# Optimization experiments

Hardware: AMD Instinct MI355X
Metric: run time of the kernel (lower is better)

The kernel has to match this reference:

```python
import jax, jax.numpy as jnp
import numpy as np

N_NODES = 50000
N_EDGES = 640000
DIM_V = 128
DIM_E = 128
BN_EPS = 1e-5


def _lrelu(x):
    return jax.nn.leaky_relu(x, 0.2)


def _mlp3(x, W1, b1, W2, b2, W3, b3):
    h = _lrelu(x @ W1 + b1)
    h = _lrelu(h @ W2 + b2)
    return h @ W3 + b3


def _bn_train(x, gamma, beta):
    # BatchNorm1d in training mode: batch stats, biased variance
    m = jnp.mean(x, axis=0)
    v = jnp.mean((x - m) ** 2, axis=0)
    return (x - m) * jax.lax.rsqrt(v + BN_EPS) * gamma + beta


def setup_inputs() -> dict:
    key = jax.random.key(0)
    ks = jax.random.split(key, 20)
    node_fea = jax.random.normal(ks[0], (N_NODES, DIM_V), dtype=jnp.float32)
    edge_fea = jax.random.normal(ks[1], (N_EDGES, DIM_E), dtype=jnp.float32)
    idx1 = jax.random.randint(ks[2], (N_EDGES,), 0, N_NODES)
    idx2 = jax.random.randint(ks[3], (N_EDGES,), 0, N_NODES)
    dt_e = 2 * DIM_V + DIM_E  # phi_e input dim
    dt_v = DIM_V + DIM_E      # phi_v input dim
    s = 0.05
    return {
        "node_fea": node_fea, "edge_fea": edge_fea,
        "idx1": idx1, "idx2": idx2,
        "We1": jax.random.normal(ks[4], (dt_e, DIM_E), jnp.float32) * s,
        "be1": jnp.zeros((DIM_E,), jnp.float32),
        "We2": jax.random.normal(ks[5], (DIM_E, DIM_E), jnp.float32) * s,
        "be2": jnp.zeros((DIM_E,), jnp.float32),
        "We3": jax.random.normal(ks[6], (DIM_E, DIM_E), jnp.float32) * s,
        "be3": jnp.zeros((DIM_E,), jnp.float32),
        "Wv1": jax.random.normal(ks[7], (dt_v, DIM_V), jnp.float32) * s,
        "bv1": jnp.zeros((DIM_V,), jnp.float32),
        "Wv2": jax.random.normal(ks[8], (DIM_V, DIM_V), jnp.float32) * s,
        "bv2": jnp.zeros((DIM_V,), jnp.float32),
        "Wv3": jax.random.normal(ks[9], (DIM_V, DIM_V), jnp.float32) * s,
        "bv3": jnp.zeros((DIM_V,), jnp.float32),
        "gamma_e": jnp.ones((DIM_E,), jnp.float32),
        "beta_e": jnp.zeros((DIM_E,), jnp.float32),
        "gamma_v": jnp.ones((DIM_V,), jnp.float32),
        "beta_v": jnp.zeros((DIM_V,), jnp.float32),
    }


def reference(node_fea, edge_fea, idx1, idx2,
              We1, be1, We2, be2, We3, be3,
              Wv1, bv1, Wv2, bv2, Wv3, bv3,
              gamma_e, beta_e, gamma_v, beta_v):
    n_nodes = node_fea.shape[0]
    # gather endpoints, concat with edge features -> [E, 2*dim_v + dim_e]
    z = jnp.concatenate([node_fea[idx1], node_fea[idx2], edge_fea], axis=1)
    ek_prime = _bn_train(_mlp3(z, We1, be1, We2, be2, We3, be3), gamma_e, beta_e)
    edge_new = edge_fea + ek_prime
    # scatter_mean over idx1 into [N, dim_v]; empty segments stay zero
    seg_sum = jax.ops.segment_sum(ek_prime, idx1, num_segments=n_nodes)
    cnt = jax.ops.segment_sum(jnp.ones((idx1.shape[0], 1), ek_prime.dtype), idx1,
                              num_segments=n_nodes)
    vi_e_bar = seg_sum / jnp.maximum(cnt, 1.0)
    z2 = jnp.concatenate([vi_e_bar, node_fea], axis=1)
    vi_prime = _bn_train(_mlp3(z2, Wv1, bv1, Wv2, bv2, Wv3, bv3), gamma_v, beta_v)
    node_new = node_fea + vi_prime
    return node_new, edge_new
```

## Files before the change

### kernel.cpp

```cpp
#include <hip/hip_runtime.h>
#include <cstddef>

#define BN_EPS 1e-5f
constexpr int NNODES = 50000;
constexpr int NEDGES = 640000;
constexpr int DV = 128;
constexpr int NSLOT_E = 512;
constexpr int NSLOT_V = 256;

typedef __attribute__((ext_vector_type(4))) float f32x4;
typedef __attribute__((ext_vector_type(8))) short s16x8;
typedef unsigned short ushort_t;

__device__ __forceinline__ float lrelu(float x) { return x > 0.f ? x : 0.2f * x; }

__device__ __forceinline__ unsigned cvt_pk_bf16(float lo, float hi) {
  unsigned r;
  asm("v_cvt_pk_bf16_f32 %0, %1, %2" : "=v"(r) : "v"(lo), "v"(hi));
  return r;
}
__device__ __forceinline__ ushort_t f2bf(float f) {
  unsigned r;
  asm("v_cvt_pk_bf16_f32 %0, %1, %1" : "=v"(r) : "v"(f));
  return (ushort_t)r;
}
__device__ __forceinline__ s16x8 pack8(float4 a, float4 b) {
  union { unsigned u[4]; s16x8 v; } r;
  r.u[0] = cvt_pk_bf16(a.x, a.y);
  r.u[1] = cvt_pk_bf16(a.z, a.w);
  r.u[2] = cvt_pk_bf16(b.x, b.y);
  r.u[3] = cvt_pk_bf16(b.z, b.w);
  return r.v;
}
__device__ __forceinline__ float bf2f(ushort_t u) {
  return __builtin_bit_cast(float, (unsigned int)u << 16);
}

__global__ __launch_bounds__(256)
void to_bf16(const float* __restrict__ src, ushort_t* __restrict__ dst, int n8) {
  int i = blockIdx.x * 256 + threadIdx.x;
  if (i >= n8) return;
  const float* s = src + (size_t)i * 8;
  float4 x0 = *(const float4*)s;
  float4 x1 = *(const float4*)(s + 4);
  *(s16x8*)(dst + (size_t)i * 8) = pack8(x0, x1);
}

__global__ __launch_bounds__(256)
void pack_all(const float* __restrict__ W0, const float* __restrict__ W1,
              const float* __restrict__ W2, const float* __restrict__ W3,
              const float* __restrict__ W4, const float* __restrict__ W5,
              ushort_t* __restrict__ out) {
  int t = blockIdx.x * 256 + threadIdx.x;
  if (t >= 288 * 64) return;
  int lane = t & 63, f = t >> 6;
  const float* W; int lf;
  if (f < 96)       { W = W0; lf = f; }
  else if (f < 128) { W = W1; lf = f - 96; }
  else if (f < 160) { W = W2; lf = f - 128; }
  else if (f < 224) { W = W3; lf = f - 160; }
  else if (f < 256) { W = W4; lf = f - 224; }
  else              { W = W5; lf = f - 256; }
  int kk = lf >> 3, n = lf & 7;
  int k0 = kk * 32 + (lane >> 4) * 8, col = n * 16 + (lane & 15);
  s16x8 v;
#pragma unroll
  for (int j = 0; j < 8; j++) v[j] = (short)f2bf(W[(size_t)(k0 + j) * DV + col]);
  *(s16x8*)(out + (size_t)t * 8) = v;
}

__global__ __launch_bounds__(256)
void csr_hist(const int* __restrict__ idx1, int* __restrict__ deg) {
  int e = blockIdx.x * 256 + threadIdx.x;
  if (e < NEDGES) atomicAdd(&deg[idx1[e]], 1);
}

__global__ __launch_bounds__(256)
void csr_scan(const int* __restrict__ deg, int* __restrict__ row_ptr,
              int* __restrict__ cursor) {
  __shared__ int part[256];
  const int t = threadIdx.x;
  const int CH = (NNODES + 255) / 256;
  int s = 0;
  for (int i = 0; i < CH; i++) { int n = t * CH + i; if (n < NNODES) s += deg[n]; }
  part[t] = s;
  __syncthreads();
  if (t == 0) {
    int run = 0;
    for (int i = 0; i < 256; i++) { int v = part[i]; part[i] = run; run += v; }
  }
  __syncthreads();
  int run = part[t];
  for (int i = 0; i < CH; i++) {
    int n = t * CH + i;
    if (n < NNODES) { row_ptr[n] = run; cursor[n] = run; run += deg[n]; }
  }
}

__global__ __launch_bounds__(256)
void csr_fill(const int* __restrict__ idx1, int* __restrict__ cursor,
              int* __restrict__ eidx) {
  int e = blockIdx.x * 256 + threadIdx.x;
  if (e < NEDGES) {
    int pos = atomicAdd(&cursor[idx1[e]], 1);
    eidx[pos] = e;
  }
}

template<int RS>
__device__ __forceinline__ void mfma_span(const char* Als, const s16x8* __restrict__ Wp,
                                          int fkk0, int nkk, f32x4 acc[2][2],
                                          int lane, int rg, int nh) {
  const int col0 = lane & 15;
  const int kg16 = (lane >> 4) * 16;
  const int sw = (col0 & 7) << 4;
  const int r0 = (rg * 32 + col0) * RS;
  const int r1 = (rg * 32 + 16 + col0) * RS;
#pragma unroll
  for (int kk = 0; kk < nkk; kk++) {
    const int ko = (kk * 64 + kg16) ^ sw;
    s16x8 a0 = *(const s16x8*)(Als + r0 + ko);
    s16x8 a1 = *(const s16x8*)(Als + r1 + ko);
    s16x8 b0 = Wp[(size_t)((fkk0 + kk) * 8 + nh * 2 + 0) * 64 + lane];
    s16x8 b1 = Wp[(size_t)((fkk0 + kk) * 8 + nh * 2 + 1) * 64 + lane];
    acc[0][0] = __builtin_amdgcn_mfma_f32_16x16x32_bf16(a0, b0, acc[0][0], 0, 0, 0);
    acc[0][1] = __builtin_amdgcn_mfma_f32_16x16x32_bf16(a0, b1, acc[0][1], 0, 0, 0);
    acc[1][0] = __builtin_amdgcn_mfma_f32_16x16x32_bf16(a1, b0, acc[1][0], 0, 0, 0);
    acc[1][1] = __builtin_amdgcn_mfma_f32_16x16x32_bf16(a1, b1, acc[1][1], 0, 0, 0);
  }
}

__device__ __forceinline__ void store_h64(char* H, const f32x4 acc[2][2],
                                          const float* __restrict__ bias,
                                          int lane, int rg, int nh) {
  const int col0 = lane & 15, lg = lane >> 4;
#pragma unroll
  for (int ar = 0; ar < 2; ar++) {
#pragma unroll
    for (int n = 0; n < 2; n++) {
      const int col = nh * 32 + n * 16 + col0;
      float bi = bias[col];
#pragma unroll
      for (int r = 0; r < 4; r++) {
        int row = rg * 32 + ar * 16 + lg * 4 + r;
        float v = lrelu(acc[ar][n][r] + bi);
        *(ushort_t*)(H + row * 256 + ((col * 2) ^ ((row & 7) << 4))) = f2bf(v);
      }
    }
  }
}

__global__ __launch_bounds__(512, 8)
void edge_mlp_mfma(const ushort_t* __restrict__ node_b, const float* __restrict__ edge_fea,
                   const int* __restrict__ idx1, const int* __restrict__ idx2,
                   const ushort_t* __restrict__ Wp1, const float* __restrict__ b1,
                   const ushort_t* __restrict__ Wp2, const float* __restrict__ b2,
                   const ushort_t* __restrict__ Wp3, const float* __restrict__ b3,
                   ushort_t* __restrict__ slot, float* __restrict__ slots) {
  __shared__ __align__(16) char zsm[64 * 384];
  __shared__ __align__(16) char hb[64 * 256];
  const int tid = threadIdx.x;
  const int lane = tid & 63, wid = tid >> 6;
  const int rg = wid & 1, nh = wid >> 1;
  const int e0 = blockIdx.x * 64;

  for (int t = tid; t < 64 * 24; t += 512) {
    int e = t / 24, p = t % 24;
    int er = e0 + e;
    const ushort_t* src = (p < 16) ? (node_b + (size_t)idx1[er] * DV + p * 8)
                                   : (node_b + (size_t)idx2[er] * DV + (p - 16) * 8);
    s16x8 v = *(const s16x8*)src;
    *(s16x8*)(zsm + e * 384 + ((p * 16) ^ ((e & 7) << 4))) = v;
  }
  __syncthreads();

  f32x4 acc[2][2];
#pragma unroll
  for (int i = 0; i < 2; i++)
#pragma unroll
    for (int j = 0; j < 2; j++) acc[i][j] = 0.0f;

  mfma_span<384>(zsm, (const s16x8*)Wp1, 0, 6, acc, lane, rg, nh);
  __syncthreads();

  for (int t = tid; t < 64 * 24; t += 512) {
    int e = t / 24, p = t % 24;
    int er = e0 + e;
    s16x8 v;
    if (p < 8) {
      v = *(const s16x8*)(node_b + (size_t)idx2[er] * DV + 64 + p * 8);
    } else {
      const float* s = edge_fea + (size_t)er * DV + (p - 8) * 8;
      float4 x0 = *(const float4*)s;
      float4 x1 = *(const float4*)(s + 4);
      v = pack8(x0, x1);
      *(s16x8*)(slot + (size_t)er * 256 + 128 + (p - 8) * 8) = v;
    }
    *(s16x8*)(zsm + e * 384 + ((p * 16) ^ ((e & 7) << 4))) = v;
  }
  __syncthreads();

  mfma_span<384>(zsm, (const s16x8*)Wp1, 6, 6, acc, lane, rg, nh);

  store_h64(hb, acc, b1, lane, rg, nh);
  __syncthreads();

#pragma unroll
  for (int i = 0; i < 2; i++)
#pragma unroll
    for (int j = 0; j < 2; j++) acc[i][j] = 0.0f;
  mfma_span<256>(hb, (const s16x8*)Wp2, 0, 4, acc, lane, rg, nh);

  store_h64(zsm, acc, b2, lane, rg, nh);
  __syncthreads();

#pragma unroll
  for (int i = 0; i < 2; i++)
#pragma unroll
    for (int j = 0; j < 2; j++) acc[i][j] = 0.0f;
  mfma_span<256>(zsm, (const s16x8*)Wp3, 0, 4, acc, lane, rg, nh);

  const int col0 = lane & 15, lg = lane >> 4;
  float* ps = (float*)hb;
  float* pq = ps + 16 * DV;
#pragma unroll
  for (int ar = 0; ar < 2; ar++) {
#pragma unroll
    for (int n = 0; n < 2; n++) {
      const int col = nh * 32 + n * 16 + col0;
      float bi = b3[col];
      float s = 0.f, q = 0.f;
#pragma unroll
      for (int r = 0; r < 4; r++) {
        int row = rg * 32 + ar * 16 + lg * 4 + r;
        float v = acc[ar][n][r] + bi;
        slot[(size_t)(e0 + row) * 256 + col] = f2bf(v);
        s += v; q += v * v;
      }
      ps[(rg * 8 + ar * 4 + lg) * DV + col] = s;
      pq[(rg * 8 + ar * 4 + lg) * DV + col] = q;
    }
  }
  __syncthreads();
  if (tid < 128) {
    float s = 0.f, q = 0.f;
#pragma unroll
    for (int g = 0; g < 16; g++) { s += ps[g * DV + tid]; q += pq[g * DV + tid]; }
    float* sl = slots + (size_t)(blockIdx.x % NSLOT_E) * 256;
    atomicAdd(sl + tid, s);
    atomicAdd(sl + 128 + tid, q);
  }
}

__global__ __launch_bounds__(256)
void node_gather_fused(const int* __restrict__ row_ptr, const int* __restrict__ deg,
                       const int* __restrict__ eidx, const float* __restrict__ ss,
                       float* eslot, ushort_t* __restrict__ vbar_b) {
  const int n = blockIdx.x * 4 + (threadIdx.x >> 6);
  const int lane = threadIdx.x & 63;
  if (n >= NNODES) return;
  const int start = row_ptr[n], d = deg[n];
  const int j = lane * 2;
  const float sc0 = ss[j], sc1 = ss[j + 1];
  const float sh0 = ss[128 + j], sh1 = ss[129 + j];
  const ushort_t* slot = (const ushort_t*)eslot;
  float a0 = 0.f, a1 = 0.f;
  int i = 0;
  for (; i + 2 <= d; i += 2) {
    int e0 = eidx[start + i], e1 = eidx[start + i + 1];
    ushort2 uh0 = *(const ushort2*)(slot + (size_t)e0 * 256 + j);
    ushort2 ue0 = *(const ushort2*)(slot + (size_t)e0 * 256 + 128 + j);
    ushort2 uh1 = *(const ushort2*)(slot + (size_t)e1 * 256 + j);
    ushort2 ue1 = *(const ushort2*)(slot + (size_t)e1 * 256 + 128 + j);
    float h00 = bf2f(uh0.x), h01 = bf2f(uh0.y);
    float h10 = bf2f(uh1.x), h11 = bf2f(uh1.y);
    a0 += h00 + h10; a1 += h01 + h11;
    float2 o0, o1;
    o0.x = bf2f(ue0.x) + fmaf(h00, sc0, sh0); o0.y = bf2f(ue0.y) + fmaf(h01, sc1, sh1);
    o1.x = bf2f(ue1.x) + fmaf(h10, sc0, sh0); o1.y = bf2f(ue1.y) + fmaf(h11, sc1, sh1);
    *(float2*)(eslot + (size_t)e0 * DV + j) = o0;
    *(float2*)(eslot + (size_t)e1 * DV + j) = o1;
  }
  if (i < d) {
    int e0 = eidx[start + i];
    ushort2 uh0 = *(const ushort2*)(slot + (size_t)e0 * 256 + j);
    ushort2 ue0 = *(const ushort2*)(slot + (size_t)e0 * 256 + 128 + j);
    float h00 = bf2f(uh0.x), h01 = bf2f(uh0.y);
    a0 += h00; a1 += h01;
    float2 o0;
    o0.x = bf2f(ue0.x) + fmaf(h00, sc0, sh0); o0.y = bf2f(ue0.y) + fmaf(h01, sc1, sh1);
    *(float2*)(eslot + (size_t)e0 * DV + j) = o0;
  }
  float vx, vy;
  if (d > 0) {
    float inv = 1.f / (float)d;
    vx = fmaf(a0 * inv, sc0, sh0);
    vy = fmaf(a1 * inv, sc1, sh1);
  } else {
    vx = 0.f; vy = 0.f;
  }
  unsigned vb = cvt_pk_bf16(vx, vy);
  *(unsigned*)(vbar_b + (size_t)n * DV + j) = vb;
}

template<int K>
__device__ __forceinline__ void layer_mfma(const char* Als, const s16x8* __restrict__ Wp,
                                           f32x4 acc[4], int lane, int rg, int nh) {
  const int arow = rg * 16 + (lane & 15);
  const int rowoff = arow * (K * 2);
  const int kg16 = (lane >> 4) * 16;
  const int sw = (arow & 7) << 4;
#pragma unroll
  for (int n = 0; n < 4; n++) acc[n] = 0.0f;
#pragma unroll 2
  for (int kk = 0; kk < K / 32; kk++) {
    s16x8 a = *(const s16x8*)(Als + rowoff + ((kk * 64 + kg16) ^ sw));
#pragma unroll
    for (int n = 0; n < 4; n++) {
      s16x8 b = Wp[(size_t)(kk * 8 + nh * 4 + n) * 64 + lane];
      acc[n] = __builtin_amdgcn_mfma_f32_16x16x32_bf16(a, b, acc[n], 0, 0, 0);
    }
  }
}

__device__ __forceinline__ void store_h_lds(char* H, const f32x4 acc[4],
                                            const float* __restrict__ bias,
                                            int lane, int rg, int nh) {
  const int col0 = lane & 15, lg = lane >> 4;
#pragma unroll
  for (int n = 0; n < 4; n++) {
    const int col = nh * 64 + n * 16 + col0;
    float bi = bias[col];
#pragma unroll
    for (int r = 0; r < 4; r++) {
      int row = rg * 16 + lg * 4 + r;
      float v = lrelu(acc[n][r] + bi);
      *(ushort_t*)(H + row * 256 + ((col * 2) ^ ((row & 7) << 4))) = f2bf(v);
    }
  }
}

__global__ __launch_bounds__(256)
void node_mlp_mfma(const ushort_t* __restrict__ node_b, const ushort_t* __restrict__ vbar_b,
                   const ushort_t* __restrict__ Wp1, const float* __restrict__ b1,
                   const ushort_t* __restrict__ Wp2, const float* __restrict__ b2,
                   const ushort_t* __restrict__ Wp3, const float* __restrict__ b3,
                   float* __restrict__ h_out, float* __restrict__ slots) {
  __shared__ __align__(16) char zsm[32 * 512];
  __shared__ __align__(16) char hb[32 * 256];
  const int tid = threadIdx.x;
  const int lane = tid & 63, wid = tid >> 6;
  const int rg = wid & 1, nh = wid >> 1;
  const int n0 = blockIdx.x * 32;

  for (int t = tid; t < 32 * 32; t += 256) {
    int e = t / 32, p = t % 32;
    int nr = n0 + e;
    s16x8 v = (s16x8)0;
    if (nr < NNODES) {
      const ushort_t* src = (p < 16) ? (vbar_b + (size_t)nr * DV + p * 8)
                                     : (node_b + (size_t)nr * DV + (p - 16) * 8);
      v = *(const s16x8*)src;
    }
    *(s16x8*)(zsm + e * 512 + ((p * 16) ^ ((e & 7) << 4))) = v;
  }
  __syncthreads();

  f32x4 acc[4];

  layer_mfma<256>(zsm, (const s16x8*)Wp1, acc, lane, rg, nh);
  store_h_lds(hb, acc, b1, lane, rg, nh);
  __syncthreads();

  layer_mfma<128>(hb, (const s16x8*)Wp2, acc, lane, rg, nh);
  __syncthreads();
  store_h_lds(zsm, acc, b2, lane, rg, nh);
  __syncthreads();

  layer_mfma<128>(zsm, (const s16x8*)Wp3, acc, lane, rg, nh);

  const int col0 = lane & 15, lg = lane >> 4;
  float* ps = (float*)hb;
  float* pq = (float*)zsm;
#pragma unroll
  for (int n = 0; n < 4; n++) {
    const int col = nh * 64 + n * 16 + col0;
    float bi = b3[col];
    float s = 0.f, q = 0.f;
#pragma unroll
    for (int r = 0; r < 4; r++) {
      int row = rg * 16 + lg * 4 + r;
      int gr = n0 + row;
      if (gr < NNODES) {
        float v = acc[n][r] + bi;
        h_out[(size_t)gr * DV + col] = v;
        s += v; q += v * v;
      }
    }
    ps[(rg * 4 + lg) * DV + col] = s;
    pq[(rg * 4 + lg) * DV + col] = q;
  }
  __syncthreads();
  if (tid < 128) {
    float s = 0.f, q = 0.f;
#pragma unroll
    for (int g = 0; g < 8; g++) { s += ps[g * DV + tid]; q += pq[g * DV + tid]; }
    float* sl = slots + (size_t)(blockIdx.x % NSLOT_V) * 256;
    atomicAdd(sl + tid, s);
    atomicAdd(sl + 128 + tid, q);
  }
}

__global__ __launch_bounds__(256)
void stats_reduce(const float* __restrict__ slots, int nslot, float inv_n,
                  const float* __restrict__ gamma, const float* __restrict__ beta,
                  float* __restrict__ ss) {
  __shared__ float tot[256];
  const int j = threadIdx.x;
  float s = 0.f;
  for (int t = 0; t < nslot; t++) s += slots[(size_t)t * 256 + j];
  tot[j] = s;
  __syncthreads();
  if (j < 128) {
    float mean = tot[j] * inv_n;
    float var = tot[j + 128] * inv_n - mean * mean;
    float rs = rsqrtf(var + BN_EPS);
    float sc = gamma[j] * rs;
    ss[j] = sc;
    ss[128 + j] = beta[j] - mean * sc;
  }
}

__global__ __launch_bounds__(256)
void node_finalize(const float* __restrict__ node_fea, const float* __restrict__ ss,
                   float* __restrict__ h_inout) {
  const size_t base = (size_t)blockIdx.x * 1024 + threadIdx.x * 4;
  const int j = (int)(base & 127);
  float4 h = *(float4*)&h_inout[base];
  float4 nf = *(const float4*)&node_fea[base];
  float4 o;
  o.x = nf.x + fmaf(h.x, ss[j + 0], ss[128 + j + 0]);
  o.y = nf.y + fmaf(h.y, ss[j + 1], ss[128 + j + 1]);
  o.z = nf.z + fmaf(h.z, ss[j + 2], ss[128 + j + 2]);
  o.w = nf.w + fmaf(h.w, ss[j + 3], ss[128 + j + 3]);
  *(float4*)&h_inout[base] = o;
}

extern "C" void kernel_launch(void* const* d_in, const int* in_sizes, int n_in,
                              void* d_out, int out_size, void* d_ws, size_t ws_size,
                              hipStream_t stream) {
  const float* node_fea = (const float*)d_in[0];
  const float* edge_fea = (const float*)d_in[1];
  const int* idx1 = (const int*)d_in[2];
  const int* idx2 = (const int*)d_in[3];
  const float* We1 = (const float*)d_in[4];  const float* be1 = (const float*)d_in[5];
  const float* We2 = (const float*)d_in[6];  const float* be2 = (const float*)d_in[7];
  const float* We3 = (const float*)d_in[8];  const float* be3 = (const float*)d_in[9];
  const float* Wv1 = (const float*)d_in[10]; const float* bv1 = (const float*)d_in[11];
  const float* Wv2 = (const float*)d_in[12]; const float* bv2 = (const float*)d_in[13];
  const float* Wv3 = (const float*)d_in[14]; const float* bv3 = (const float*)d_in[15];
  const float* gamma_e = (const float*)d_in[16]; const float* beta_e = (const float*)d_in[17];
  const float* gamma_v = (const float*)d_in[18]; const float* beta_v = (const float*)d_in[19];

  float* out_node = (float*)d_out;
  float* out_edge = out_node + (size_t)NNODES * DV;

  float* ws = (float*)d_ws;
  size_t o = 0;
  int* deg = (int*)(ws + o);      o += NNODES;
  float* slots_e = ws + o;        o += (size_t)NSLOT_E * 256;
  float* slots_v = ws + o;        o += (size_t)NSLOT_V * 256;
  const size_t zero_bytes = o * sizeof(float);
  int* row_ptr = (int*)(ws + o);  o += NNODES;
  int* cursor = (int*)(ws + o);   o += NNODES;
  int* eidx = (int*)(ws + o);     o += NEDGES;
  float* ss_e = ws + o;           o += 256;
  float* ss_v = ws + o;           o += 256;
  ushort_t* node_b = (ushort_t*)(ws + o);  o += (size_t)NNODES * DV / 2;
  ushort_t* vbar_b = (ushort_t*)(ws + o);  o += (size_t)NNODES * DV / 2;
  ushort_t* wpack = (ushort_t*)(ws + o);

  const ushort_t* Wp_e1 = wpack;
  const ushort_t* Wp_e2 = wpack + (size_t)96 * 512;
  const ushort_t* Wp_e3 = wpack + (size_t)128 * 512;
  const ushort_t* Wp_v1 = wpack + (size_t)160 * 512;
  const ushort_t* Wp_v2 = wpack + (size_t)224 * 512;
  const ushort_t* Wp_v3 = wpack + (size_t)256 * 512;

  hipMemsetAsync(d_ws, 0, zero_bytes, stream);

  to_bf16<<<(NNODES * DV / 8 + 255) / 256, 256, 0, stream>>>(node_fea, node_b, NNODES * DV / 8);
  pack_all<<<72, 256, 0, stream>>>(We1, We2, We3, Wv1, Wv2, Wv3, wpack);
  csr_hist<<<(NEDGES + 255) / 256, 256, 0, stream>>>(idx1, deg);
  csr_scan<<<1, 256, 0, stream>>>(deg, row_ptr, cursor);
  csr_fill<<<(NEDGES + 255) / 256, 256, 0, stream>>>(idx1, cursor, eidx);

  edge_mlp_mfma<<<NEDGES / 64, 512, 0, stream>>>(node_b, edge_fea, idx1, idx2,
                                                 Wp_e1, be1, Wp_e2, be2, Wp_e3, be3,
                                                 (ushort_t*)out_edge, slots_e);
  stats_reduce<<<1, 256, 0, stream>>>(slots_e, NSLOT_E, 1.f / NEDGES, gamma_e, beta_e, ss_e);
  node_gather_fused<<<(NNODES + 3) / 4, 256, 0, stream>>>(row_ptr, deg, eidx,
                                                          ss_e, out_edge, vbar_b);
  node_mlp_mfma<<<(NNODES + 31) / 32, 256, 0, stream>>>(node_b, vbar_b,
                                                        Wp_v1, bv1, Wp_v2, bv2, Wp_v3, bv3,
                                                        out_node, slots_v);
  stats_reduce<<<1, 256, 0, stream>>>(slots_v, NSLOT_V, 1.f / NNODES, gamma_v, beta_v, ss_v);
  node_finalize<<<(NNODES * DV) / 1024, 256, 0, stream>>>(node_fea, ss_v, out_node);
}
```

Baseline: 859.7 us.

## Split edge finalize into streaming kernel, gather only h3 in node pass

The bf16 copy of edge_fea is no longer written into the output slot by the edge MLP. The node gather now reads only the h3 half with a 4-way unrolled loop to build the scatter-mean. A new streaming kernel then re-reads edge_fea in fp32 and writes edge_new in edge order rather than as random per-node scattered writes. This trades scattered read-modify-write traffic for an extra coalesced pass and one more kernel launch.

```diff
diff --git a/kernel.cpp b/kernel.cpp
--- a/kernel.cpp
+++ b/kernel.cpp
@@ -156,7 +156,7 @@
                    const ushort_t* __restrict__ Wp1, const float* __restrict__ b1,
                    const ushort_t* __restrict__ Wp2, const float* __restrict__ b2,
                    const ushort_t* __restrict__ Wp3, const float* __restrict__ b3,
-                   ushort_t* __restrict__ slot, float* __restrict__ slots) {
+                   ushort_t* __restrict__ h3b, float* __restrict__ slots) {
   __shared__ __align__(16) char zsm[64 * 384];
   __shared__ __align__(16) char hb[64 * 256];
   const int tid = threadIdx.x;
@@ -194,7 +194,6 @@
       float4 x0 = *(const float4*)s;
       float4 x1 = *(const float4*)(s + 4);
       v = pack8(x0, x1);
-      *(s16x8*)(slot + (size_t)er * 256 + 128 + (p - 8) * 8) = v;
     }
     *(s16x8*)(zsm + e * 384 + ((p * 16) ^ ((e & 7) << 4))) = v;
   }
@@ -234,7 +233,7 @@
       for (int r = 0; r < 4; r++) {
         int row = rg * 32 + ar * 16 + lg * 4 + r;
         float v = acc[ar][n][r] + bi;
-        slot[(size_t)(e0 + row) * 256 + col] = f2bf(v);
+        h3b[(size_t)(e0 + row) * 256 + col] = f2bf(v);
         s += v; q += v * v;
       }
       ps[(rg * 8 + ar * 4 + lg) * DV + col] = s;
@@ -253,54 +252,56 @@
 }
 
 __global__ __launch_bounds__(256)
-void node_gather_fused(const int* __restrict__ row_ptr, const int* __restrict__ deg,
-                       const int* __restrict__ eidx, const float* __restrict__ ss,
-                       float* eslot, ushort_t* __restrict__ vbar_b) {
+void node_gather(const int* __restrict__ row_ptr, const int* __restrict__ deg,
+                 const int* __restrict__ eidx, const float* __restrict__ ss,
+                 const ushort_t* __restrict__ h3b, ushort_t* __restrict__ vbar_b) {
   const int n = blockIdx.x * 4 + (threadIdx.x >> 6);
   const int lane = threadIdx.x & 63;
   if (n >= NNODES) return;
   const int start = row_ptr[n], d = deg[n];
   const int j = lane * 2;
-  const float sc0 = ss[j], sc1 = ss[j + 1];
-  const float sh0 = ss[128 + j], sh1 = ss[129 + j];
-  const ushort_t* slot = (const ushort_t*)eslot;
   float a0 = 0.f, a1 = 0.f;
   int i = 0;
-  for (; i + 2 <= d; i += 2) {
+  for (; i + 4 <= d; i += 4) {
     int e0 = eidx[start + i], e1 = eidx[start + i + 1];
-    ushort2 uh0 = *(const ushort2*)(slot + (size_t)e0 * 256 + j);
-    ushort2 ue0 = *(const ushort2*)(slot + (size_t)e0 * 256 + 128 + j);
-    ushort2 uh1 = *(const ushort2*)(slot + (size_t)e1 * 256 + j);
-    ushort2 ue1 = *(const ushort2*)(slot + (size_t)e1 * 256 + 128 + j);
-    float h00 = bf2f(uh0.x), h01 = bf2f(uh0.y);
-    float h10 = bf2f(uh1.x), h11 = bf2f(uh1.y);
-    a0 += h00 + h10; a1 += h01 + h11;
-    float2 o0, o1;
-    o0.x = bf2f(ue0.x) + fmaf(h00, sc0, sh0); o0.y = bf2f(ue0.y) + fmaf(h01, sc1, sh1);
-    o1.x = bf2f(ue1.x) + fmaf(h10, sc0, sh0); o1.y = bf2f(ue1.y) + fmaf(h11, sc1, sh1);
-    *(float2*)(eslot + (size_t)e0 * DV + j) = o0;
-    *(float2*)(eslot + (size_t)e1 * DV + j) = o1;
-  }
-  if (i < d) {
+    int e2 = eidx[start + i + 2], e3 = eidx[start + i + 3];
+    ushort2 u0 = *(const ushort2*)(h3b + (size_t)e0 * 256 + j);
+    ushort2 u1 = *(const ushort2*)(h3b + (size_t)e1 * 256 + j);
+    ushort2 u2 = *(const ushort2*)(h3b + (size_t)e2 * 256 + j);
+    ushort2 u3 = *(const ushort2*)(h3b + (size_t)e3 * 256 + j);
+    a0 += (bf2f(u0.x) + bf2f(u1.x)) + (bf2f(u2.x) + bf2f(u3.x));
+    a1 += (bf2f(u0.y) + bf2f(u1.y)) + (bf2f(u2.y) + bf2f(u3.y));
+  }
+  for (; i < d; i++) {
     int e0 = eidx[start + i];
-    ushort2 uh0 = *(const ushort2*)(slot + (size_t)e0 * 256 + j);
-    ushort2 ue0 = *(const ushort2*)(slot + (size_t)e0 * 256 + 128 + j);
-    float h00 = bf2f(uh0.x), h01 = bf2f(uh0.y);
-    a0 += h00; a1 += h01;
-    float2 o0;
-    o0.x = bf2f(ue0.x) + fmaf(h00, sc0, sh0); o0.y = bf2f(ue0.y) + fmaf(h01, sc1, sh1);
-    *(float2*)(eslot + (size_t)e0 * DV + j) = o0;
+    ushort2 u0 = *(const ushort2*)(h3b + (size_t)e0 * 256 + j);
+    a0 += bf2f(u0.x); a1 += bf2f(u0.y);
   }
   float vx, vy;
   if (d > 0) {
     float inv = 1.f / (float)d;
-    vx = fmaf(a0 * inv, sc0, sh0);
-    vy = fmaf(a1 * inv, sc1, sh1);
+    vx = fmaf(a0 * inv, ss[j], ss[128 + j]);
+    vy = fmaf(a1 * inv, ss[j + 1], ss[129 + j]);
   } else {
     vx = 0.f; vy = 0.f;
   }
   unsigned vb = cvt_pk_bf16(vx, vy);
   *(unsigned*)(vbar_b + (size_t)n * DV + j) = vb;
+}
+
+__global__ __launch_bounds__(256)
+void edge_finalize_stream(const float* __restrict__ edge_fea, const float* __restrict__ ss,
+                          float* eslot) {
+  const int e = blockIdx.x * 4 + (threadIdx.x >> 6);
+  const int lane = threadIdx.x & 63;
+  const int j = lane * 2;
+  const ushort_t* h3b = (const ushort_t*)eslot;
+  ushort2 uh = *(const ushort2*)(h3b + (size_t)e * 256 + j);
+  float2 f = *(const float2*)(edge_fea + (size_t)e * DV + j);
+  float2 o;
+  o.x = f.x + fmaf(bf2f(uh.x), ss[j], ss[128 + j]);
+  o.y = f.y + fmaf(bf2f(uh.y), ss[j + 1], ss[129 + j]);
+  *(float2*)(eslot + (size_t)e * DV + j) = o;
 }
 
 template<int K>
@@ -499,8 +500,9 @@
                                                  Wp_e1, be1, Wp_e2, be2, Wp_e3, be3,
                                                  (ushort_t*)out_edge, slots_e);
   stats_reduce<<<1, 256, 0, stream>>>(slots_e, NSLOT_E, 1.f / NEDGES, gamma_e, beta_e, ss_e);
-  node_gather_fused<<<(NNODES + 3) / 4, 256, 0, stream>>>(row_ptr, deg, eidx,
-                                                          ss_e, out_edge, vbar_b);
+  node_gather<<<(NNODES + 3) / 4, 256, 0, stream>>>(row_ptr, deg, eidx, ss_e,
+                                                    (const ushort_t*)out_edge, vbar_b);
+  edge_finalize_stream<<<NEDGES / 4, 256, 0, stream>>>(edge_fea, ss_e, out_edge);
   node_mlp_mfma<<<(NNODES + 31) / 32, 256, 0, stream>>>(node_b, vbar_b,
                                                         Wp_v1, bv1, Wp_v2, bv2, Wp_v3, bv3,
                                                         out_node, slots_v);
```

Result: slower. 893.5 us (+3.9%).
